# Kernel optimization log

Measured on AMD Instinct MI355X. Metric: run time of the kernel, lower is better.

Reference implementation:

```python
import jax, jax.numpy as jnp
import numpy as np

B, N, H, HID, LOCALITY = 2, 4096, 4, 256, 30.0
VD = HID // H
F32_MAX = jnp.finfo(jnp.float32).max


def setup_inputs() -> dict:
    key = jax.random.key(0)
    k1, k2, k3, k4 = jax.random.split(key, 4)
    m_dist = jax.random.uniform(k1, (B, N, N), dtype=jnp.float32)  # pairwise distances (b,N,N)
    x = jax.random.normal(k2, (B, N, HID), dtype=jnp.float32)
    r = jax.random.normal(k3, (1, H, 1, 1), dtype=jnp.float32)  # learned per-head distance scale
    # lecun_normal: std = 1/sqrt(fan_in), fan_in = HID
    weight = jax.random.normal(k4, (H, HID, VD), dtype=jnp.float32) / np.sqrt(HID)
    return {"m_dist": m_dist, "x": x, "r": r, "weight": weight}


def reference(m_dist, x, r, weight):
    # scaled distance per head: (b,h,n,n)
    scaled = m_dist[:, None, :, :] * (r ** 2)
    # percentile-thresholded local mask (linear interpolation, per row)
    thresh = jnp.percentile(scaled, LOCALITY, axis=-1, keepdims=True, method="linear")
    scaled = jnp.where(scaled <= thresh, scaled, F32_MAX)
    att = jax.nn.softmax(-scaled, axis=-1)  # (b,h,n,n)
    value = jnp.einsum("bnj,hjk->bhnk", x, weight)  # (b,h,n,v)
    out = jnp.einsum("bhnj,bhjd->bhnd", att, value)  # (b,h,n,v)
    out = jnp.transpose(out, (0, 2, 1, 3)).reshape(out.shape[0], -1, HID)  # (b,n,hid)
    return jax.nn.gelu(out, approximate=False)
```

## Files before the change

### kernel.cpp

```cpp
#include <hip/hip_runtime.h>
#include <hip/hip_bf16.h>

#define Bc   2
#define Nc   4096
#define Hc   4
#define HIDc 256
#define VDc  64

typedef short s8v  __attribute__((ext_vector_type(8)));
typedef float f4v  __attribute__((ext_vector_type(4)));

static __device__ __forceinline__ unsigned short bf16bits(float f) {
    __hip_bfloat16 h = __float2bfloat16(f);
    return *(unsigned short*)&h;
}

__global__ __launch_bounds__(256) void front_kernel(
    const float* __restrict__ m_dist, const float* __restrict__ wgt,
    unsigned short* __restrict__ wh, unsigned short* __restrict__ wl,
    float* __restrict__ thr_out, float* __restrict__ min_out)
{
    int t = threadIdx.x, bid = blockIdx.x;

    if (bid < 128) {
        int h  = bid >> 5;
        int kt = (bid >> 3) & 3;
        int jc = bid & 7;
        int lane = t >> 2, ii = t & 3;
        #pragma unroll
        for (int u = 0; u < 2; u++) {
            int i = ii * 2 + u;
            int j = jc * 32 + (lane >> 4) * 8 + i;
            int k = kt * 16 + (lane & 15);
            float v = wgt[((size_t)h * HIDc + j) * VDc + k];
            __hip_bfloat16 hb = __float2bfloat16(v);
            float hf = __bfloat162float(hb);
            size_t o = ((((size_t)h * 4 + kt) * 8 + jc) * 64 + lane) * 8 + i;
            wh[o] = *(unsigned short*)&hb;
            wl[o] = bf16bits(v - hf);
        }
        return;
    }

    __shared__ unsigned int hist[1024];
    __shared__ float wredf[4];
    __shared__ unsigned int wsum[4];
    __shared__ unsigned int wscan[4];
    __shared__ int b0s, b1s;
    __shared__ unsigned int c0s;
    __shared__ unsigned int ncand;
    __shared__ float cand[256];
    __shared__ float s0s, s1s;

    size_t rowid = bid - 128;
    const float* row = m_dist + rowid * Nc;

    float4 vals[4];
    float lmin = 1e30f;
    #pragma unroll
    for (int i = 0; i < 4; i++) {
        float4 v = ((const float4*)row)[t + i * 256];
        vals[i] = v;
        lmin = fminf(lmin, fminf(fminf(v.x, v.y), fminf(v.z, v.w)));
    }
    #pragma unroll
    for (int o = 32; o > 0; o >>= 1) lmin = fminf(lmin, __shfl_xor(lmin, o));
    if ((t & 63) == 0) wredf[t >> 6] = lmin;

    const unsigned int R0 = 1228u, R1 = 1229u;
    float wlo = 0.25f, whi = 0.35f;
    int b0 = 0, b1 = 0;
    unsigned int C0 = 0;

    for (;;) {
        float wscale = 1024.0f / (whi - wlo);

        for (int i = t; i < 1024; i += 256) hist[i] = 0u;
        if (t == 0) ncand = 0u;
        __syncthreads();

        unsigned int cb = 0;
        #pragma unroll
        for (int i = 0; i < 4; i++) {
            float a[4] = {vals[i].x, vals[i].y, vals[i].z, vals[i].w};
            #pragma unroll
            for (int j = 0; j < 4; j++) {
                float v = a[j];
                if (v < wlo) {
                    cb++;
                } else {
                    int bx = (int)((v - wlo) * wscale);
                    if (bx < 1024) atomicAdd(&hist[bx], 1u);
                }
            }
        }
        #pragma unroll
        for (int o = 32; o > 0; o >>= 1) cb += __shfl_xor(cb, o);
        if ((t & 63) == 0) wsum[t >> 6] = cb;
        __syncthreads();
        unsigned int Cb = wsum[0] + wsum[1] + wsum[2] + wsum[3];

        unsigned int c[4], csum = 0;
        #pragma unroll
        for (int j = 0; j < 4; j++) { c[j] = hist[t * 4 + j]; csum += c[j]; }
        unsigned int inc = csum;
        #pragma unroll
        for (int o = 1; o < 64; o <<= 1) {
            unsigned int nv = __shfl_up(inc, o);
            if ((t & 63) >= o) inc += nv;
        }
        if ((t & 63) == 63) wscan[t >> 6] = inc;
        __syncthreads();
        unsigned int wpref = 0;
        for (int wv = 0; wv < (t >> 6); wv++) wpref += wscan[wv];
        unsigned int T = wscan[0] + wscan[1] + wscan[2] + wscan[3];
        unsigned int P = Cb + wpref + inc - csum;

        unsigned int cum = P;
        #pragma unroll
        for (int j = 0; j < 4; j++) {
            unsigned int lo = cum, hi = cum + c[j];
            if (R0 >= lo && R0 < hi) { b0s = t * 4 + j; c0s = lo; }
            if (R1 >= lo && R1 < hi) { b1s = t * 4 + j; }
            cum = hi;
        }
        __syncthreads();

        if (Cb <= R0 && R1 < Cb + T) { b0 = b0s; b1 = b1s; C0 = c0s; break; }
        wlo = 0.0f; whi = 1.001f;
    }

    float wscale = 1024.0f / (whi - wlo);
    #pragma unroll
    for (int i = 0; i < 4; i++) {
        float a[4] = {vals[i].x, vals[i].y, vals[i].z, vals[i].w};
        #pragma unroll
        for (int j = 0; j < 4; j++) {
            float v = a[j];
            if (v >= wlo) {
                int bx = (int)((v - wlo) * wscale);
                if (bx >= b0 && bx <= b1) {
                    unsigned int p = atomicAdd(&ncand, 1u);
                    if (p < 256u) cand[p] = v;
                }
            }
        }
    }
    __syncthreads();
    unsigned int nc = min(ncand, 256u);
    if ((unsigned int)t < nc) {
        float v = cand[t];
        unsigned int rk = C0;
        for (unsigned int j = 0; j < nc; j++) {
            float u = cand[j];
            rk += (u < v || (u == v && j < (unsigned int)t)) ? 1u : 0u;
        }
        if (rk == R0) s0s = v;
        if (rk == R1) s1s = v;
    }
    __syncthreads();
    if (t == 0) {
        thr_out[rowid] = 0.5f * (s0s + s1s);
        min_out[rowid] = fminf(fminf(wredf[0], wredf[1]), fminf(wredf[2], wredf[3]));
    }
}

__global__ __launch_bounds__(256) void value_kernel(
    const float* __restrict__ x,
    const unsigned short* __restrict__ wh, const unsigned short* __restrict__ wl,
    unsigned short* __restrict__ vt_g)
{
    int t  = threadIdx.x;
    int bid = blockIdx.x;
    int nt = bid & 63;
    int h  = (bid >> 6) & 3;
    int b  = bid >> 8;
    int n0 = nt * 64;

    int w = t >> 6, lane = t & 63, q4 = lane >> 4, m16 = lane & 15;
    int nb = n0 + w * 16;

    const float* xp = x + ((size_t)(b * Nc + nb + m16)) * HIDc + q4 * 8;

    f4v acc[4];
    #pragma unroll
    for (int kt = 0; kt < 4; kt++) acc[kt] = (f4v){0.f, 0.f, 0.f, 0.f};

    #pragma unroll
    for (int jc = 0; jc < 8; jc++) {
        float4 xv0 = *(const float4*)(xp + jc * 32);
        float4 xv1 = *(const float4*)(xp + jc * 32 + 4);
        float f[8] = {xv0.x, xv0.y, xv0.z, xv0.w, xv1.x, xv1.y, xv1.z, xv1.w};
        union { s8v v; unsigned short u[8]; } hs, ls;
        #pragma unroll
        for (int i = 0; i < 8; i++) {
            __hip_bfloat16 hb = __float2bfloat16(f[i]);
            float hf = __bfloat162float(hb);
            hs.u[i] = *(unsigned short*)&hb;
            ls.u[i] = bf16bits(f[i] - hf);
        }
        #pragma unroll
        for (int kt = 0; kt < 4; kt++) {
            size_t ao = (((size_t)(h * 4 + kt) * 8 + jc) << 9) + lane * 8;
            s8v ah = *(const s8v*)(wh + ao);
            s8v al = *(const s8v*)(wl + ao);
            acc[kt] = __builtin_amdgcn_mfma_f32_16x16x32_bf16(ah, hs.v, acc[kt], 0, 0, 0);
            acc[kt] = __builtin_amdgcn_mfma_f32_16x16x32_bf16(al, hs.v, acc[kt], 0, 0, 0);
            acc[kt] = __builtin_amdgcn_mfma_f32_16x16x32_bf16(ah, ls.v, acc[kt], 0, 0, 0);
        }
    }

    unsigned short* vg = vt_g + (((size_t)b * Hc + h) * VDc) * Nc;
    #pragma unroll
    for (int kt = 0; kt < 4; kt++) {
        #pragma unroll
        for (int rg = 0; rg < 4; rg++) {
            int k = kt * 16 + q4 * 4 + rg;
            vg[(size_t)k * Nc + nb + m16] = bf16bits(acc[kt][rg]);
        }
    }
}

#define NT 64
#define JT 32
#define BIGF 3.0e38f

__global__ __launch_bounds__(1024, 8) void attn_kernel(
    const float* __restrict__ m_dist, const float* __restrict__ rr,
    const unsigned short* __restrict__ vt_g,
    const float* __restrict__ thr_g, const float* __restrict__ min_g,
    float* __restrict__ Op, float* __restrict__ Zp, int jlen)
{
    __shared__ float ms[2][NT * JT];
    __shared__ unsigned short vt[2][Hc * VDc * JT];

    int t = threadIdx.x;
    const int nblk = Bc * (Nc / NT);
    int js = blockIdx.x / nblk;
    int rb = blockIdx.x - js * nblk;
    int b  = rb >> 6;
    int n0 = (rb & 63) * NT;
    int j0 = js * jlen;

    int lane = t & 63, q = lane >> 4, m16 = lane & 15;
    int w = t >> 6;
    int h = w & 3, rq = w >> 2;
    int row = rq * 16 + m16;

    float mn = min_g[b * Nc + n0 + row];
    float rv = rr[h];
    float cc = -(rv * rv) * 1.4426950408889634f;
    float nmncc = -mn * cc;

    f4v acc[4];
    #pragma unroll
    for (int ct = 0; ct < 4; ct++) acc[ct] = (f4v){0.f, 0.f, 0.f, 0.f};
    float zacc = 0.f;

    const float* mbase = m_dist + ((size_t)b * Nc + n0) * Nc + j0;
    const unsigned short* vtb = vt_g + ((size_t)b * Hc * VDc) * Nc + j0;

    int mrow = t >> 3, mch = t & 7;
    int msw  = mrow * JT + ((mch ^ (mrow & 7)) << 2);
    const float* msrc = mbase + (size_t)mrow * Nc + mch * 4;
    float thm = (t < 512) ? thr_g[b * Nc + n0 + mrow] : 0.f;

    int vrow = t >> 2;
    int vlc  = (t & 3) ^ (vrow & 3);
    const unsigned short* vsrc = vtb + (size_t)vrow * Nc + vlc * 8;

    int s7 = m16 & 7;
    int a0o = row * JT + (((q * 2 + 0) ^ s7) << 2);
    int a1o = row * JT + (((q * 2 + 1) ^ s7) << 2);
    int bco = (q ^ (m16 & 3)) << 3;

    int niter = jlen / JT;

    float4 msreg;
    if (t < 512) msreg = *(const float4*)(msrc);
    __builtin_amdgcn_global_load_lds(
        (const __attribute__((address_space(1))) void*)(vsrc),
        (__attribute__((address_space(3))) void*)(&vt[0][(size_t)t * 8]),
        16, 0, 0);

    int cur = 0;
    for (int it = 0; it < niter; ++it) {
        if (t < 512) {
            float4 v = msreg;
            v.x = (v.x <= thm) ? v.x : BIGF;
            v.y = (v.y <= thm) ? v.y : BIGF;
            v.z = (v.z <= thm) ? v.z : BIGF;
            v.w = (v.w <= thm) ? v.w : BIGF;
            *(float4*)&ms[cur][msw] = v;
        }
        __syncthreads();

        if (it + 1 < niter) {
            int jn = (it + 1) * JT;
            if (t < 512) msreg = *(const float4*)(msrc + jn);
            __builtin_amdgcn_global_load_lds(
                (const __attribute__((address_space(1))) void*)(vsrc + jn),
                (__attribute__((address_space(3))) void*)(&vt[cur ^ 1][(size_t)t * 8]),
                16, 0, 0);
        }

        const unsigned short* vb = &vt[cur][h * VDc * JT];
        float4 a0 = *(const float4*)&ms[cur][a0o];
        float4 a1 = *(const float4*)&ms[cur][a1o];
        float w0 = __builtin_amdgcn_exp2f(__builtin_fmaf(a0.x, cc, nmncc));
        float w1 = __builtin_amdgcn_exp2f(__builtin_fmaf(a0.y, cc, nmncc));
        float w2 = __builtin_amdgcn_exp2f(__builtin_fmaf(a0.z, cc, nmncc));
        float w3 = __builtin_amdgcn_exp2f(__builtin_fmaf(a0.w, cc, nmncc));
        float w4 = __builtin_amdgcn_exp2f(__builtin_fmaf(a1.x, cc, nmncc));
        float w5 = __builtin_amdgcn_exp2f(__builtin_fmaf(a1.y, cc, nmncc));
        float w6 = __builtin_amdgcn_exp2f(__builtin_fmaf(a1.z, cc, nmncc));
        float w7 = __builtin_amdgcn_exp2f(__builtin_fmaf(a1.w, cc, nmncc));
        zacc += ((w0 + w1) + (w2 + w3)) + ((w4 + w5) + (w6 + w7));
        union { s8v v; __hip_bfloat162 h2[4]; } afu;
        afu.h2[0] = __float22bfloat162_rn((float2){w0, w1});
        afu.h2[1] = __float22bfloat162_rn((float2){w2, w3});
        afu.h2[2] = __float22bfloat162_rn((float2){w4, w5});
        afu.h2[3] = __float22bfloat162_rn((float2){w6, w7});
        #pragma unroll
        for (int ct = 0; ct < 4; ct++) {
            int brow = ct * 16 + m16;
            s8v bf = *(const s8v*)(vb + brow * JT + bco);
            acc[ct] = __builtin_amdgcn_mfma_f32_16x16x32_bf16(afu.v, bf, acc[ct], 0, 0, 0);
        }
        cur ^= 1;
    }

    zacc += __shfl_xor(zacc, 16);
    zacc += __shfl_xor(zacc, 32);
    if (q == 0)
        Zp[(((size_t)js * Bc + b) * Hc + h) * Nc + n0 + row] = zacc;

    #pragma unroll
    for (int ct = 0; ct < 4; ct++) {
        #pragma unroll
        for (int rg = 0; rg < 4; rg++) {
            int nl = rq * 16 + q * 4 + rg;
            Op[(((size_t)js * Bc + b) * Nc + n0 + nl) * HIDc + h * VDc + ct * 16 + m16]
                = acc[ct][rg];
        }
    }
}

__global__ __launch_bounds__(256) void combine_kernel(
    const float* __restrict__ Op, const float* __restrict__ Zp,
    float* __restrict__ out, int S)
{
    int g = blockIdx.x * 256 + threadIdx.x;
    int c4 = g & 63;
    int n  = (g >> 6) & (Nc - 1);
    int b  = g >> 18;
    int h  = c4 >> 4;

    float z = 0.f;
    float4 v = {0.f, 0.f, 0.f, 0.f};
    for (int s = 0; s < S; s++) {
        z += Zp[(((size_t)s * Bc + b) * Hc + h) * Nc + n];
        float4 p = *(const float4*)&Op[(((size_t)s * Bc + b) * Nc + n) * HIDc + c4 * 4];
        v.x += p.x; v.y += p.y; v.z += p.z; v.w += p.w;
    }
    float iz = 1.0f / z;
    float4 o;
    float u;
    u = v.x * iz; o.x = 0.5f * u * (1.0f + erff(u * 0.7071067811865476f));
    u = v.y * iz; o.y = 0.5f * u * (1.0f + erff(u * 0.7071067811865476f));
    u = v.z * iz; o.z = 0.5f * u * (1.0f + erff(u * 0.7071067811865476f));
    u = v.w * iz; o.w = 0.5f * u * (1.0f + erff(u * 0.7071067811865476f));
    *(float4*)&out[(((size_t)b * Nc + n) * HIDc) + c4 * 4] = o;
}

extern "C" void kernel_launch(void* const* d_in, const int* in_sizes, int n_in,
                              void* d_out, int out_size, void* d_ws, size_t ws_size,
                              hipStream_t stream) {
    const float* m_dist = (const float*)d_in[0];
    const float* x      = (const float*)d_in[1];
    const float* r      = (const float*)d_in[2];
    const float* weight = (const float*)d_in[3];
    float* out = (float*)d_out;

    char* ws = (char*)d_ws;
    const size_t MB = 1024 * 1024;
    unsigned short* vt = (unsigned short*)ws;
    float* thr = (float*)(ws + 4 * MB);
    float* mn  = (float*)(ws + 4 * MB + 32 * 1024);
    float* Zp  = (float*)(ws + 4 * MB + 64 * 1024);
    float* Op  = (float*)(ws + 5 * MB);

    const size_t OpSz = (size_t)Bc * Nc * HIDc * 4;
    int S = 4;
    if (ws_size < 6 * MB + 4 * OpSz) S = 2;
    if (ws_size < 6 * MB + 2 * OpSz) S = 1;
    int jlen = Nc / S;

    char* pb = ws + 5 * MB + (size_t)S * OpSz;
    unsigned short* wh = (unsigned short*)pb;
    unsigned short* wl = (unsigned short*)(pb + 128 * 1024);

    front_kernel<<<128 + Bc * Nc, 256, 0, stream>>>(m_dist, weight, wh, wl, thr, mn);
    value_kernel<<<512, 256, 0, stream>>>(x, wh, wl, vt);
    attn_kernel<<<S * Bc * (Nc / NT), 1024, 0, stream>>>(m_dist, r, vt, thr, mn, Op, Zp, jlen);
    combine_kernel<<<(Bc * Nc * HIDc) / 1024, 256, 0, stream>>>(Op, Zp, out, S);
}
```

Baseline: 263.1 us.

## Triple-buffer attention tiles with direct global-to-LDS loads and per-row masking

The distance tile is now loaded straight into shared memory with global_load_lds instead of being staged through registers. The threshold mask therefore moves to the consumer, which sets masked weights to zero after reading. Buffering goes from double to triple, with a two-stage prefetch and one barrier per iteration guarded by manual vmcnt waits. This cuts register staging and a barrier and gives the loads more time to overlap compute. In exchange it uses more LDS, which may lower occupancy, and it relies on hand-counted vmcnt values that differ between wave groups.

```diff
diff --git a/kernel.cpp b/kernel.cpp
--- a/kernel.cpp
+++ b/kernel.cpp
@@ -223,7 +223,6 @@
 
 #define NT 64
 #define JT 32
-#define BIGF 3.0e38f
 
 __global__ __launch_bounds__(1024, 8) void attn_kernel(
     const float* __restrict__ m_dist, const float* __restrict__ rr,
@@ -231,8 +230,8 @@
     const float* __restrict__ thr_g, const float* __restrict__ min_g,
     float* __restrict__ Op, float* __restrict__ Zp, int jlen)
 {
-    __shared__ float ms[2][NT * JT];
-    __shared__ unsigned short vt[2][Hc * VDc * JT];
+    __shared__ float msL[3][NT * JT];
+    __shared__ unsigned short vtL[3][Hc * VDc * JT];
 
     int t = threadIdx.x;
     const int nblk = Bc * (Nc / NT);
@@ -248,6 +247,7 @@
     int row = rq * 16 + m16;
 
     float mn = min_g[b * Nc + n0 + row];
+    float thm = thr_g[b * Nc + n0 + row];
     float rv = rr[h];
     float cc = -(rv * rv) * 1.4426950408889634f;
     float nmncc = -mn * cc;
@@ -260,61 +260,64 @@
     const float* mbase = m_dist + ((size_t)b * Nc + n0) * Nc + j0;
     const unsigned short* vtb = vt_g + ((size_t)b * Hc * VDc) * Nc + j0;
 
-    int mrow = t >> 3, mch = t & 7;
-    int msw  = mrow * JT + ((mch ^ (mrow & 7)) << 2);
-    const float* msrc = mbase + (size_t)mrow * Nc + mch * 4;
-    float thm = (t < 512) ? thr_g[b * Nc + n0 + mrow] : 0.f;
-
-    int vrow = t >> 2;
-    int vlc  = (t & 3) ^ (vrow & 3);
-    const unsigned short* vsrc = vtb + (size_t)vrow * Nc + vlc * 8;
+    const float* msrc = mbase + (size_t)(t >> 3) * Nc + (((t & 7) ^ ((t >> 3) & 7)) << 2);
+    const unsigned short* vsrc = vtb + (size_t)(t >> 2) * Nc + (((t & 3) ^ ((t >> 2) & 3)) << 3);
 
     int s7 = m16 & 7;
     int a0o = row * JT + (((q * 2 + 0) ^ s7) << 2);
     int a1o = row * JT + (((q * 2 + 1) ^ s7) << 2);
     int bco = (q ^ (m16 & 3)) << 3;
+    const int hoff = h * VDc * JT;
 
     int niter = jlen / JT;
 
-    float4 msreg;
-    if (t < 512) msreg = *(const float4*)(msrc);
-    __builtin_amdgcn_global_load_lds(
-        (const __attribute__((address_space(1))) void*)(vsrc),
-        (__attribute__((address_space(3))) void*)(&vt[0][(size_t)t * 8]),
-        16, 0, 0);
-
-    int cur = 0;
+    #define STAGE(k, bi) do {                                                  \
+        int jo_ = (k) * JT;                                                    \
+        if (t < 512)                                                           \
+            __builtin_amdgcn_global_load_lds(                                  \
+                (const __attribute__((address_space(1))) void*)(msrc + jo_),   \
+                (__attribute__((address_space(3))) void*)                      \
+                    ((char*)&msL[bi][0] + (size_t)t * 16),                     \
+                16, 0, 0);                                                     \
+        __builtin_amdgcn_global_load_lds(                                      \
+            (const __attribute__((address_space(1))) void*)(vsrc + jo_),       \
+            (__attribute__((address_space(3))) void*)                          \
+                ((char*)&vtL[bi][0] + (size_t)t * 16),                         \
+            16, 0, 0);                                                         \
+    } while (0)
+
+    STAGE(0, 0);
+    STAGE(1, 1);
+
+    int bi = 0;
     for (int it = 0; it < niter; ++it) {
-        if (t < 512) {
-            float4 v = msreg;
-            v.x = (v.x <= thm) ? v.x : BIGF;
-            v.y = (v.y <= thm) ? v.y : BIGF;
-            v.z = (v.z <= thm) ? v.z : BIGF;
-            v.w = (v.w <= thm) ? v.w : BIGF;
-            *(float4*)&ms[cur][msw] = v;
-        }
-        __syncthreads();
-
         if (it + 1 < niter) {
-            int jn = (it + 1) * JT;
-            if (t < 512) msreg = *(const float4*)(msrc + jn);
-            __builtin_amdgcn_global_load_lds(
-                (const __attribute__((address_space(1))) void*)(vsrc + jn),
-                (__attribute__((address_space(3))) void*)(&vt[cur ^ 1][(size_t)t * 8]),
-                16, 0, 0);
-        }
-
-        const unsigned short* vb = &vt[cur][h * VDc * JT];
-        float4 a0 = *(const float4*)&ms[cur][a0o];
-        float4 a1 = *(const float4*)&ms[cur][a1o];
-        float w0 = __builtin_amdgcn_exp2f(__builtin_fmaf(a0.x, cc, nmncc));
-        float w1 = __builtin_amdgcn_exp2f(__builtin_fmaf(a0.y, cc, nmncc));
-        float w2 = __builtin_amdgcn_exp2f(__builtin_fmaf(a0.z, cc, nmncc));
-        float w3 = __builtin_amdgcn_exp2f(__builtin_fmaf(a0.w, cc, nmncc));
-        float w4 = __builtin_amdgcn_exp2f(__builtin_fmaf(a1.x, cc, nmncc));
-        float w5 = __builtin_amdgcn_exp2f(__builtin_fmaf(a1.y, cc, nmncc));
-        float w6 = __builtin_amdgcn_exp2f(__builtin_fmaf(a1.z, cc, nmncc));
-        float w7 = __builtin_amdgcn_exp2f(__builtin_fmaf(a1.w, cc, nmncc));
+            if (w < 8) { asm volatile("s_waitcnt vmcnt(2)" ::: "memory"); }
+            else       { asm volatile("s_waitcnt vmcnt(1)" ::: "memory"); }
+        } else {
+            asm volatile("s_waitcnt vmcnt(0)" ::: "memory");
+        }
+        __builtin_amdgcn_sched_barrier(0);
+        __builtin_amdgcn_s_barrier();
+        __builtin_amdgcn_sched_barrier(0);
+
+        if (it + 2 < niter) {
+            int bn = bi + 2; if (bn >= 3) bn -= 3;
+            STAGE(it + 2, bn);
+        }
+
+        const float* msp = &msL[bi][0];
+        const unsigned short* vb = &vtL[bi][hoff];
+        float4 a0 = *(const float4*)(msp + a0o);
+        float4 a1 = *(const float4*)(msp + a1o);
+        float w0 = (a0.x <= thm) ? __builtin_amdgcn_exp2f(__builtin_fmaf(a0.x, cc, nmncc)) : 0.f;
+        float w1 = (a0.y <= thm) ? __builtin_amdgcn_exp2f(__builtin_fmaf(a0.y, cc, nmncc)) : 0.f;
+        float w2 = (a0.z <= thm) ? __builtin_amdgcn_exp2f(__builtin_fmaf(a0.z, cc, nmncc)) : 0.f;
+        float w3 = (a0.w <= thm) ? __builtin_amdgcn_exp2f(__builtin_fmaf(a0.w, cc, nmncc)) : 0.f;
+        float w4 = (a1.x <= thm) ? __builtin_amdgcn_exp2f(__builtin_fmaf(a1.x, cc, nmncc)) : 0.f;
+        float w5 = (a1.y <= thm) ? __builtin_amdgcn_exp2f(__builtin_fmaf(a1.y, cc, nmncc)) : 0.f;
+        float w6 = (a1.z <= thm) ? __builtin_amdgcn_exp2f(__builtin_fmaf(a1.z, cc, nmncc)) : 0.f;
+        float w7 = (a1.w <= thm) ? __builtin_amdgcn_exp2f(__builtin_fmaf(a1.w, cc, nmncc)) : 0.f;
         zacc += ((w0 + w1) + (w2 + w3)) + ((w4 + w5) + (w6 + w7));
         union { s8v v; __hip_bfloat162 h2[4]; } afu;
         afu.h2[0] = __float22bfloat162_rn((float2){w0, w1});
@@ -327,8 +330,9 @@
             s8v bf = *(const s8v*)(vb + brow * JT + bco);
             acc[ct] = __builtin_amdgcn_mfma_f32_16x16x32_bf16(afu.v, bf, acc[ct], 0, 0, 0);
         }
-        cur ^= 1;
-    }
+        bi = bi + 1; if (bi >= 3) bi -= 3;
+    }
+    #undef STAGE
 
     zacc += __shfl_xor(zacc, 16);
     zacc += __shfl_xor(zacc, 32);
```

New measurement: 263.4 us. No clear change (+0.1%).
